# Kernel tuning notes

Hardware: AMD Instinct MI355X
Metric: run time of the kernel (lower is better)

## Reference

```python
import jax, jax.numpy as jnp
import numpy as np
import math

N, D, H = 4096, 2048, 16
HD = D // H  # head_dim = 128


def setup_inputs() -> dict:
    key = jax.random.key(0)
    ks = jax.random.split(key, 9)
    s = 1.0 / math.sqrt(D)
    return {
        "x":  jax.random.normal(ks[0], (N, D), dtype=jnp.float32),
        "Wq": jax.random.normal(ks[1], (D, D), dtype=jnp.float32) * s,
        "bq": jax.random.normal(ks[2], (D,), dtype=jnp.float32) * s,
        "Wk": jax.random.normal(ks[3], (D, D), dtype=jnp.float32) * s,
        "bk": jax.random.normal(ks[4], (D,), dtype=jnp.float32) * s,
        "Wv": jax.random.normal(ks[5], (D, D), dtype=jnp.float32) * s,
        "bv": jax.random.normal(ks[6], (D,), dtype=jnp.float32) * s,
        "Wo": jax.random.normal(ks[7], (D, D), dtype=jnp.float32) * s,
        "bo": jax.random.normal(ks[8], (D,), dtype=jnp.float32) * s,
    }


def reference(x, Wq, bq, Wk, bk, Wv, bv, Wo, bo):
    # eqx.nn.Linear: y = W @ x + b, weight shape (out, in) -> x @ W.T + b
    q = x @ Wq.T + bq            # [N, D]
    k = x @ Wk.T + bk            # [N, D]
    v = x @ Wv.T + bv            # [N, D]
    q = q.reshape(N, H, HD).transpose(1, 0, 2)   # [H, N, hd]
    k = k.reshape(N, H, HD).transpose(1, 2, 0)   # [H, hd, N]
    v = v.reshape(N, H, HD).transpose(1, 0, 2)   # [H, N, hd]
    scale = 1.0 / math.sqrt(HD)
    scores = jnp.matmul(q * scale, k)            # [H, N, N]
    attn = jax.nn.softmax(scores, axis=-1)
    ctx = jnp.matmul(attn, v)                    # [H, N, hd]
    ctx = ctx.transpose(1, 0, 2).reshape(N, D)   # [N, D]
    return ctx @ Wo.T + bo
```

## Files before the change

### kernel.cpp

```cpp
#include <hip/hip_runtime.h>
#include <stdint.h>

#define N_TOK 4096
#define DIM   2048
#define NH    16
#define HD    128
#define NW    (DIM * DIM)

using bf16x8 = __attribute__((ext_vector_type(8))) short;
using bf16x4 = __attribute__((ext_vector_type(4))) short;
using f32x4  = __attribute__((ext_vector_type(4))) float;

#if __has_builtin(__builtin_amdgcn_exp2f)
#define EXP2(x) __builtin_amdgcn_exp2f(x)
#else
#define EXP2(x) exp2f(x)
#endif

__device__ inline unsigned short f2bf(float f) {
  union { float f; unsigned u; } v; v.f = f;
  unsigned r = v.u + 0x7FFFu + ((v.u >> 16) & 1u);
  return (unsigned short)(r >> 16);
}
__device__ inline float bf2f(unsigned short u) {
  union { unsigned u; float f; } v; v.u = ((unsigned)u) << 16; return v.f;
}
__device__ inline f32x4 mfma16(bf16x8 a, bf16x8 b, f32x4 c) {
  return __builtin_amdgcn_mfma_f32_16x16x32_bf16(a, b, c, 0, 0, 0);
}
__device__ inline void gll16(const unsigned short* g, unsigned short* l) {
  __builtin_amdgcn_global_load_lds(
      (const __attribute__((address_space(1))) void*)g,
      (__attribute__((address_space(3))) void*)l, 16, 0, 0);
}

__global__ __launch_bounds__(256)
void cvt_bf16(const float* __restrict__ src, unsigned short* __restrict__ dst, int n) {
  int i = blockIdx.x * 256 + threadIdx.x;
  if (i * 8 >= n) return;
  const float4* s = (const float4*)src + (size_t)i * 2;
  float4 a = s[0], b = s[1];
  bf16x8 o;
  o[0] = (short)f2bf(a.x); o[1] = (short)f2bf(a.y);
  o[2] = (short)f2bf(a.z); o[3] = (short)f2bf(a.w);
  o[4] = (short)f2bf(b.x); o[5] = (short)f2bf(b.y);
  o[6] = (short)f2bf(b.z); o[7] = (short)f2bf(b.w);
  *(bf16x8*)(dst + (size_t)i * 8) = o;
}

template<int OUT_MODE>
__global__ __launch_bounds__(256)
void gemm_bf16(const unsigned short* __restrict__ A, const unsigned short* __restrict__ B,
               const float* __restrict__ bias, void* __restrict__ out_, float scale) {
  __shared__ unsigned short Asl[128 * 32];
  __shared__ unsigned short Bsl[128 * 32];
  const int tid  = threadIdx.x;
  const int lane = tid & 63, w = tid >> 6;
  const int wy = w >> 1, wx = w & 1;
  const int lr = lane & 15, quad = lane >> 4;
  const int m0 = blockIdx.y * 128, n0 = blockIdx.x * 128;

  const f32x4 vzero = {0.f, 0.f, 0.f, 0.f};
  f32x4 acc[4][4];
#pragma unroll
  for (int i = 0; i < 4; ++i)
#pragma unroll
    for (int j = 0; j < 4; ++j) acc[i][j] = vzero;

  for (int k0 = 0; k0 < DIM; k0 += 32) {
    __syncthreads();
#pragma unroll
    for (int i = 0; i < 2; ++i) {
      int ch = tid + i * 256;
      int r = ch >> 2, cc = ch & 3;
      gll16(&A[(size_t)(m0 + r) * DIM + k0 + cc * 8], &Asl[ch * 8]);
      gll16(&B[(size_t)(n0 + r) * DIM + k0 + cc * 8], &Bsl[ch * 8]);
    }
    __syncthreads();

    bf16x8 af[4], bfv[4];
#pragma unroll
    for (int mb = 0; mb < 4; ++mb)
      af[mb] = *(const bf16x8*)&Asl[(wy * 64 + mb * 16 + lr) * 32 + quad * 8];
#pragma unroll
    for (int nb = 0; nb < 4; ++nb)
      bfv[nb] = *(const bf16x8*)&Bsl[(wx * 64 + nb * 16 + lr) * 32 + quad * 8];
#pragma unroll
    for (int mb = 0; mb < 4; ++mb)
#pragma unroll
      for (int nb = 0; nb < 4; ++nb)
        acc[mb][nb] = mfma16(af[mb], bfv[nb], acc[mb][nb]);
  }

#pragma unroll
  for (int mb = 0; mb < 4; ++mb)
#pragma unroll
    for (int nb = 0; nb < 4; ++nb) {
      int gn = n0 + wx * 64 + nb * 16 + lr;
      int gm_base = m0 + wy * 64 + mb * 16 + quad * 4;
      float bs = bias[gn];
      if constexpr (OUT_MODE == 2) {
        bf16x4 pk;
#pragma unroll
        for (int r = 0; r < 4; ++r) pk[r] = (short)f2bf((acc[mb][nb][r] + bs) * scale);
        *(bf16x4*)&((unsigned short*)out_)[(size_t)gn * N_TOK + gm_base] = pk;
      } else {
#pragma unroll
        for (int r = 0; r < 4; ++r) {
          float v = (acc[mb][nb][r] + bs) * scale;
          if constexpr (OUT_MODE == 1)
            ((float*)out_)[(size_t)(gm_base + r) * DIM + gn] = v;
          else
            ((unsigned short*)out_)[(size_t)(gm_base + r) * DIM + gn] = f2bf(v);
        }
      }
    }
}

__global__ __launch_bounds__(256)
void flash_attn(const unsigned short* __restrict__ Q,
                const unsigned short* __restrict__ K,
                const unsigned short* __restrict__ Vt,
                unsigned short* __restrict__ ctx) {
  constexpr int LDK = 136;
  constexpr int LDV = 72;
  constexpr int LDP = 72;
  __shared__ unsigned short Ksl[64 * LDK];
  __shared__ unsigned short VTsl[128 * LDV];
  __shared__ unsigned short Psl[4][32 * LDP];

  const int tid  = threadIdx.x;
  const int lane = tid & 63, w = tid >> 6;
  const int lr = lane & 15, quad = lane >> 4;
  const int hoff = blockIdx.y * HD;
  const int q0   = blockIdx.x * 128;
  const int qw   = q0 + w * 32;

  bf16x8 qf[2][4];
#pragma unroll
  for (int mb = 0; mb < 2; ++mb)
#pragma unroll
    for (int c = 0; c < 4; ++c)
      qf[mb][c] = *(const bf16x8*)&Q[(size_t)(qw + mb * 16 + lr) * DIM + hoff + c * 32 + quad * 8];

  const f32x4 vzero = {0.f, 0.f, 0.f, 0.f};
  f32x4 o[2][8];
  float l_part[2][4];
#pragma unroll
  for (int mb = 0; mb < 2; ++mb) {
#pragma unroll
    for (int nb = 0; nb < 8; ++nb) o[mb][nb] = vzero;
#pragma unroll
    for (int r = 0; r < 4; ++r) l_part[mb][r] = 0.f;
  }

  bf16x8 kreg[4], vreg[4];
  auto load_tile = [&](int kt) {
    int kbase = kt * 64;
#pragma unroll
    for (int i = 0; i < 4; ++i) {
      int ch = tid + i * 256;
      kreg[i] = *(const bf16x8*)&K[(size_t)(kbase + (ch >> 4)) * DIM + hoff + (ch & 15) * 8];
      vreg[i] = *(const bf16x8*)&Vt[(size_t)(hoff + (ch >> 3)) * N_TOK + kbase + (ch & 7) * 8];
    }
  };
  load_tile(0);

  for (int kt = 0; kt < N_TOK / 64; ++kt) {
    __syncthreads();
#pragma unroll
    for (int i = 0; i < 4; ++i) {
      int ch = tid + i * 256;
      *(bf16x8*)&Ksl[(ch >> 4) * LDK + (ch & 15) * 8] = kreg[i];
      *(bf16x8*)&VTsl[(ch >> 3) * LDV + (ch & 7) * 8] = vreg[i];
    }
    __syncthreads();
    if (kt + 1 < N_TOK / 64) load_tile(kt + 1);

    f32x4 s[2][4];
#pragma unroll
    for (int mb = 0; mb < 2; ++mb)
#pragma unroll
      for (int nf = 0; nf < 4; ++nf) s[mb][nf] = vzero;
#pragma unroll
    for (int nf = 0; nf < 4; ++nf)
#pragma unroll
      for (int c = 0; c < 4; ++c) {
        bf16x8 kf = *(const bf16x8*)&Ksl[(nf * 16 + lr) * LDK + c * 32 + quad * 8];
#pragma unroll
        for (int mb = 0; mb < 2; ++mb) s[mb][nf] = mfma16(qf[mb][c], kf, s[mb][nf]);
      }

#pragma unroll
    for (int mb = 0; mb < 2; ++mb)
#pragma unroll
      for (int nf = 0; nf < 4; ++nf)
#pragma unroll
        for (int r = 0; r < 4; ++r) {
          unsigned short us = f2bf(EXP2(s[mb][nf][r]));
          l_part[mb][r] += bf2f(us);
          Psl[w][(mb * 16 + quad * 4 + r) * LDP + nf * 16 + lr] = us;
        }
    __asm__ volatile("s_waitcnt lgkmcnt(0)" ::: "memory");

    bf16x8 pf[2][2];
#pragma unroll
    for (int mb = 0; mb < 2; ++mb)
#pragma unroll
      for (int ki = 0; ki < 2; ++ki)
        pf[mb][ki] = *(const bf16x8*)&Psl[w][(mb * 16 + lr) * LDP + ki * 32 + quad * 8];

#pragma unroll
    for (int nb = 0; nb < 8; ++nb)
#pragma unroll
      for (int ki = 0; ki < 2; ++ki) {
        bf16x8 vf = *(const bf16x8*)&VTsl[(nb * 16 + lr) * LDV + ki * 32 + quad * 8];
#pragma unroll
        for (int mb = 0; mb < 2; ++mb) o[mb][nb] = mfma16(pf[mb][ki], vf, o[mb][nb]);
      }
  }

#pragma unroll
  for (int mb = 0; mb < 2; ++mb)
#pragma unroll
    for (int r = 0; r < 4; ++r) {
      float t = l_part[mb][r];
      t += __shfl_xor(t, 1);
      t += __shfl_xor(t, 2);
      t += __shfl_xor(t, 4);
      t += __shfl_xor(t, 8);
      float inv = 1.0f / t;
      int gq = qw + mb * 16 + quad * 4 + r;
#pragma unroll
      for (int nb = 0; nb < 8; ++nb)
        ctx[(size_t)gq * DIM + hoff + nb * 16 + lr] = f2bf(o[mb][nb][r] * inv);
    }
}

extern "C" void kernel_launch(void* const* d_in, const int* in_sizes, int n_in,
                              void* d_out, int out_size, void* d_ws, size_t ws_size,
                              hipStream_t stream) {
  (void)in_sizes; (void)n_in; (void)out_size; (void)ws_size;
  const float* x  = (const float*)d_in[0];
  const float* Wq = (const float*)d_in[1];
  const float* bq = (const float*)d_in[2];
  const float* Wk = (const float*)d_in[3];
  const float* bk = (const float*)d_in[4];
  const float* Wv = (const float*)d_in[5];
  const float* bv = (const float*)d_in[6];
  const float* Wo = (const float*)d_in[7];
  const float* bo = (const float*)d_in[8];

  const size_t NE = (size_t)N_TOK * DIM;
  unsigned short* xb  = (unsigned short*)d_ws;
  unsigned short* Wqb = xb + NE;
  unsigned short* Wkb = Wqb + NW;
  unsigned short* Wvb = Wkb + NW;
  unsigned short* Wob = Wvb + NW;
  unsigned short* Qb  = Wob + NW;
  unsigned short* Kb  = Qb + NE;
  unsigned short* Vtb = Kb + NE;

  cvt_bf16<<<4096, 256, 0, stream>>>(x,  xb,  (int)NE);
  cvt_bf16<<<2048, 256, 0, stream>>>(Wq, Wqb, NW);
  cvt_bf16<<<2048, 256, 0, stream>>>(Wk, Wkb, NW);
  cvt_bf16<<<2048, 256, 0, stream>>>(Wv, Wvb, NW);
  cvt_bf16<<<2048, 256, 0, stream>>>(Wo, Wob, NW);

  dim3 gemm_grid(DIM / 128, N_TOK / 128);
  const float qscale = 1.4426950408889634f * 0.08838834764831845f;

  gemm_bf16<0><<<gemm_grid, 256, 0, stream>>>(xb, Wqb, bq, Qb, qscale);
  gemm_bf16<0><<<gemm_grid, 256, 0, stream>>>(xb, Wkb, bk, Kb, 1.0f);
  gemm_bf16<2><<<gemm_grid, 256, 0, stream>>>(xb, Wvb, bv, Vtb, 1.0f);

  unsigned short* ctxb = xb;
  flash_attn<<<dim3(N_TOK / 128, NH), 256, 0, stream>>>(Qb, Kb, Vtb, ctxb);

  gemm_bf16<1><<<gemm_grid, 256, 0, stream>>>(ctxb, Wob, bo, (float*)d_out, 1.0f);
}
```

Baseline: 524.0 us.

## Keep attention probabilities in registers via transposed QK and permlane swaps

The QK^T MFMA now runs with operands swapped, so each lane holds scores along the key dimension for a single query row. The exp'd probabilities are packed to bf16 with v_cvt_pk_bf16_f32 and rearranged into the PV A-operand layout using permlane32/16 swaps, which removes the per-wave LDS staging buffer, its stores, the lgkmcnt wait and the reloads. The row-sum is now accumulated per lane in fp32 and reduced across lane groups only at the end, and it is no longer rounded to bf16 to match P exactly. Correctness depends on the permlane lane mapping matching the MFMA operand layout.

```diff
diff --git a/kernel.cpp b/kernel.cpp
--- a/kernel.cpp
+++ b/kernel.cpp
@@ -10,6 +10,7 @@
 using bf16x8 = __attribute__((ext_vector_type(8))) short;
 using bf16x4 = __attribute__((ext_vector_type(4))) short;
 using f32x4  = __attribute__((ext_vector_type(4))) float;
+using u32x2  = __attribute__((ext_vector_type(2))) unsigned int;
 
 #if __has_builtin(__builtin_amdgcn_exp2f)
 #define EXP2(x) __builtin_amdgcn_exp2f(x)
@@ -32,6 +33,39 @@
   __builtin_amdgcn_global_load_lds(
       (const __attribute__((address_space(1))) void*)g,
       (__attribute__((address_space(3))) void*)l, 16, 0, 0);
+}
+
+__device__ inline unsigned cvtpk_bf16(float lo, float hi) {
+  unsigned r;
+  asm("v_cvt_pk_bf16_f32 %0, %1, %2" : "=v"(r) : "v"(lo), "v"(hi));
+  return r;
+}
+
+__device__ inline u32x2 pl32swap(unsigned a, unsigned b) {
+#if __has_builtin(__builtin_amdgcn_permlane32_swap)
+  return __builtin_amdgcn_permlane32_swap(a, b, false, false);
+#else
+  int lane = threadIdx.x & 63;
+  unsigned as = (unsigned)__shfl_xor((int)a, 32);
+  unsigned bs = (unsigned)__shfl_xor((int)b, 32);
+  u32x2 r;
+  r.x = (lane & 32) ? bs : a;
+  r.y = (lane & 32) ? b : as;
+  return r;
+#endif
+}
+__device__ inline u32x2 pl16swap(unsigned a, unsigned b) {
+#if __has_builtin(__builtin_amdgcn_permlane16_swap)
+  return __builtin_amdgcn_permlane16_swap(a, b, false, false);
+#else
+  int lane = threadIdx.x & 63;
+  unsigned as = (unsigned)__shfl_xor((int)a, 16);
+  unsigned bs = (unsigned)__shfl_xor((int)b, 16);
+  u32x2 r;
+  r.x = (lane & 16) ? bs : a;
+  r.y = (lane & 16) ? b : as;
+  return r;
+#endif
 }
 
 __global__ __launch_bounds__(256)
@@ -124,10 +158,8 @@
                 unsigned short* __restrict__ ctx) {
   constexpr int LDK = 136;
   constexpr int LDV = 72;
-  constexpr int LDP = 72;
   __shared__ unsigned short Ksl[64 * LDK];
   __shared__ unsigned short VTsl[128 * LDV];
-  __shared__ unsigned short Psl[4][32 * LDP];
 
   const int tid  = threadIdx.x;
   const int lane = tid & 63, w = tid >> 6;
@@ -145,14 +177,11 @@
 
   const f32x4 vzero = {0.f, 0.f, 0.f, 0.f};
   f32x4 o[2][8];
-  float l_part[2][4];
-#pragma unroll
-  for (int mb = 0; mb < 2; ++mb) {
+  float l_acc[2] = {0.f, 0.f};
+#pragma unroll
+  for (int mb = 0; mb < 2; ++mb)
 #pragma unroll
     for (int nb = 0; nb < 8; ++nb) o[mb][nb] = vzero;
-#pragma unroll
-    for (int r = 0; r < 4; ++r) l_part[mb][r] = 0.f;
-  }
 
   bf16x8 kreg[4], vreg[4];
   auto load_tile = [&](int kt) {
@@ -188,27 +217,36 @@
       for (int c = 0; c < 4; ++c) {
         bf16x8 kf = *(const bf16x8*)&Ksl[(nf * 16 + lr) * LDK + c * 32 + quad * 8];
 #pragma unroll
-        for (int mb = 0; mb < 2; ++mb) s[mb][nf] = mfma16(qf[mb][c], kf, s[mb][nf]);
-      }
-
-#pragma unroll
-    for (int mb = 0; mb < 2; ++mb)
-#pragma unroll
-      for (int nf = 0; nf < 4; ++nf)
-#pragma unroll
-        for (int r = 0; r < 4; ++r) {
-          unsigned short us = f2bf(EXP2(s[mb][nf][r]));
-          l_part[mb][r] += bf2f(us);
-          Psl[w][(mb * 16 + quad * 4 + r) * LDP + nf * 16 + lr] = us;
-        }
-    __asm__ volatile("s_waitcnt lgkmcnt(0)" ::: "memory");
+        for (int mb = 0; mb < 2; ++mb) s[mb][nf] = mfma16(kf, qf[mb][c], s[mb][nf]);
+      }
 
     bf16x8 pf[2][2];
 #pragma unroll
-    for (int mb = 0; mb < 2; ++mb)
-#pragma unroll
-      for (int ki = 0; ki < 2; ++ki)
-        pf[mb][ki] = *(const bf16x8*)&Psl[w][(mb * 16 + lr) * LDP + ki * 32 + quad * 8];
+    for (int mb = 0; mb < 2; ++mb) {
+      unsigned W[4][2];
+      float lp = 0.f;
+#pragma unroll
+      for (int nf = 0; nf < 4; ++nf) {
+        float e0 = EXP2(s[mb][nf][0]);
+        float e1 = EXP2(s[mb][nf][1]);
+        float e2 = EXP2(s[mb][nf][2]);
+        float e3 = EXP2(s[mb][nf][3]);
+        lp += (e0 + e1) + (e2 + e3);
+        W[nf][0] = cvtpk_bf16(e0, e1);
+        W[nf][1] = cvtpk_bf16(e2, e3);
+      }
+      l_acc[mb] += lp;
+#pragma unroll
+      for (int ki = 0; ki < 2; ++ki) {
+        u32x2 a0  = pl32swap(W[2 * ki][0], W[2 * ki + 1][0]);
+        u32x2 t02 = pl16swap(a0.x, a0.y);
+        u32x2 a1  = pl32swap(W[2 * ki][1], W[2 * ki + 1][1]);
+        u32x2 t13 = pl16swap(a1.x, a1.y);
+        union { unsigned u[4]; bf16x8 v; } pu;
+        pu.u[0] = t02.x; pu.u[1] = t13.x; pu.u[2] = t02.y; pu.u[3] = t13.y;
+        pf[mb][ki] = pu.v;
+      }
+    }
 
 #pragma unroll
     for (int nb = 0; nb < 8; ++nb)
@@ -221,15 +259,18 @@
   }
 
 #pragma unroll
+  for (int mb = 0; mb < 2; ++mb) {
+    float t = l_acc[mb];
+    t += __shfl_xor(t, 16);
+    t += __shfl_xor(t, 32);
+    l_acc[mb] = t;
+  }
+#pragma unroll
   for (int mb = 0; mb < 2; ++mb)
 #pragma unroll
     for (int r = 0; r < 4; ++r) {
-      float t = l_part[mb][r];
-      t += __shfl_xor(t, 1);
-      t += __shfl_xor(t, 2);
-      t += __shfl_xor(t, 4);
-      t += __shfl_xor(t, 8);
-      float inv = 1.0f / t;
+      float Lr = __shfl(l_acc[mb], quad * 4 + r);
+      float inv = 1.0f / Lr;
       int gq = qw + mb * 16 + quad * 4 + r;
 #pragma unroll
       for (int nb = 0; nb < 8; ++nb)
```

New measurement: 491.6 us. -6.2%, faster.
